# Kernel tuning notes

Measured on AMD Instinct MI355X. Metric: run time of the kernel, lower is better.

## Reference

```python
import jax, jax.numpy as jnp
import numpy as np

PATCH_WEIGHT = 0.5  # module init kwarg
B, C, H = 2, 4, 128  # vol dims (H=W=D)
N, P = 128, 32       # num patches total, patch edge (Hp=Wp=Dp)


def setup_inputs() -> dict:
    key = jax.random.key(0)
    k1, k2, k3 = jax.random.split(key, 3)
    patches = jax.random.normal(k1, (N, C, P, P, P), dtype=jnp.float32)
    vol = jax.random.normal(k2, (B, C, H, H, H), dtype=jnp.float32)
    # lower bound in [0, H-P] so the PxPxP slice stays in-bounds; center = lower + P//2
    crop_centers = jax.random.randint(k3, (N, 3), 0, H - P + 1, dtype=jnp.int32) + P // 2
    return {"patches": patches, "vol": vol, "crop_centers": crop_centers}


def reference(patches, vol, crop_centers):
    n, c_dim, p = patches.shape[0], patches.shape[1], patches.shape[2]
    b_dim = vol.shape[0]
    num_patch_per_batch = n // b_dim
    b_idx = jnp.arange(n) // num_patch_per_batch            # [N] batch index per patch
    lo = crop_centers - p // 2                              # [N,3] slice lower bounds
    offs = jnp.arange(p)
    hi = lo[:, 0, None] + offs                              # [N,P]
    wi = lo[:, 1, None] + offs                              # [N,P]
    di = lo[:, 2, None] + offs                              # [N,P]
    c_idx = jnp.arange(c_dim)
    # module: new_vol = vol*(1-pw); w_t is overwritten with ones, so add pw*patch
    new_vol = vol * (1.0 - PATCH_WEIGHT)
    new_vol = new_vol.at[
        b_idx[:, None, None, None, None],
        c_idx[None, :, None, None, None],
        hi[:, None, :, None, None],
        wi[:, None, None, :, None],
        di[:, None, None, None, :],
    ].add(patches * PATCH_WEIGHT)                           # scatter-add handles overlaps
    return new_vol
```

## Files before the change

### kernel.cpp

```cpp
#include <hip/hip_runtime.h>


#define PW 0.5f
constexpr int C = 4, H = 128, P = 32;
constexpr int NPB = 64;
constexpr int PCH = P * P * P;

__global__ __launch_bounds__(256) void patch_gather_kernel(
        const float* __restrict__ patches,
        const int*   __restrict__ centers,
        const float4* __restrict__ vol4,
        float4* __restrict__ out4) {
    __shared__ int s_list[NPB];
    __shared__ int s_n;

    int blk = blockIdx.x;
    int b   = blk >> 11;
    int blo = blk & 2047;
    int tid = threadIdx.x;

    int h  = blo >> 4;
    int w0 = (blo << 3) & 127;

    if (tid < 64) {
        int pn  = tid;
        int lo0 = centers[(b * NPB + pn) * 3 + 0] - 16;
        int lo1 = centers[(b * NPB + pn) * 3 + 1] - 16;
        int lo2 = centers[(b * NPB + pn) * 3 + 2] - 16;
        bool hit = ((unsigned)(h - lo0) < P) &&
                   ((unsigned)(w0 - lo1 + 7) < (P + 7));
        unsigned long long m = __ballot(hit);
        if (hit) {
            int pos = __popcll(m & ((1ull << tid) - 1ull));
            s_list[pos] = (pn << 21) | (lo0 << 14) | (lo1 << 7) | lo2;
        }
        if (tid == 0) s_n = __popcll(m);
    }
    __syncthreads();

    int d0 = (tid & 31) * 4;
    int w  = w0 + (tid >> 5);

    float acc[C][4] = {};
    int nh = s_n;
    const float* pbatch = patches + (size_t)b * NPB * C * PCH;

    for (int i = 0; i < nh; ++i) {
        int e   = s_list[i];
        int pn  = e >> 21;
        int lo1 = (e >> 7) & 127;
        unsigned wi = (unsigned)(w - lo1);
        if (wi < P) {
            int lo0 = (e >> 14) & 127;
            int lo2 = e & 127;
            int hi  = h - lo0;
            int k0  = d0 - lo2;
            if (k0 > -4 && k0 < P) {
                const float* pb = pbatch + (size_t)pn * C * PCH
                                + hi * (P * P) + wi * P;
                #pragma unroll
                for (int e4 = 0; e4 < 4; ++e4) {
                    int k = k0 + e4;
                    if ((unsigned)k < P) {
                        #pragma unroll
                        for (int c = 0; c < C; ++c)
                            acc[c][e4] += pb[c * PCH + k];
                    }
                }
            }
        }
    }

    #pragma unroll
    for (int c = 0; c < C; ++c) {
        int idx4 = ((((b * C + c) * H + h) * H + w) * H + d0) >> 2;
        float4 v = vol4[idx4];
        float4 o;
        o.x = v.x * (1.0f - PW) + acc[c][0] * PW;
        o.y = v.y * (1.0f - PW) + acc[c][1] * PW;
        o.z = v.z * (1.0f - PW) + acc[c][2] * PW;
        o.w = v.w * (1.0f - PW) + acc[c][3] * PW;
        out4[idx4] = o;
    }
}

extern "C" void kernel_launch(void* const* d_in, const int* in_sizes, int n_in,
                              void* d_out, int out_size, void* d_ws, size_t ws_size,
                              hipStream_t stream) {
    const float* patches = (const float*)d_in[0];
    const float* vol     = (const float*)d_in[1];
    const int*   centers = (const int*)d_in[2];
    float* out = (float*)d_out;

    patch_gather_kernel<<<4096, 256, 0, stream>>>(
        patches, centers, (const float4*)vol, (float4*)out);
}
```

Measured before the change: 53.63 us.

## Scatter patch rows into shared-memory accumulator with float4 loads and LDS atomics

Instead of each thread scanning every hit patch and doing scalar, divergent gathers, each hit patch's overlapping rows are loaded with coalesced float4 reads and scattered into a per-block shared-memory accumulator using LDS atomicAdd. The patch list entries now carry precomputed h/w offsets and width count so only overlapping rows are processed. Volume loads are issued early to overlap with the scatter phase. This adds a shared-memory zeroing pass, an extra barrier, and LDS atomic contention on unaligned d offsets.

```diff
diff --git a/kernel.cpp b/kernel.cpp
--- a/kernel.cpp
+++ b/kernel.cpp
@@ -1,16 +1,16 @@
 #include <hip/hip_runtime.h>
 
 
-#define PW 0.5f
-constexpr int C = 4, H = 128, P = 32;
 constexpr int NPB = 64;
-constexpr int PCH = P * P * P;
+constexpr int CH4 = 128 * 128 * 32;
+constexpr int PCH4 = 32 * 32 * 8;
 
 __global__ __launch_bounds__(256) void patch_gather_kernel(
-        const float* __restrict__ patches,
+        const float4* __restrict__ patches4,
         const int*   __restrict__ centers,
         const float4* __restrict__ vol4,
         float4* __restrict__ out4) {
+    __shared__ float s_acc[4 * 8 * 128];
     __shared__ int s_list[NPB];
     __shared__ int s_n;
 
@@ -22,65 +22,73 @@
     int h  = blo >> 4;
     int w0 = (blo << 3) & 127;
 
+    int base4 = (((b * 4) * 128 + h) * 128 + (w0 + (tid >> 5))) * 32 + (tid & 31);
+    float4 v0 = vol4[base4];
+    float4 v1 = vol4[base4 + CH4];
+    float4 v2 = vol4[base4 + 2 * CH4];
+    float4 v3 = vol4[base4 + 3 * CH4];
+
+    float4* sa4 = (float4*)s_acc;
+    #pragma unroll
+    for (int j = 0; j < 4; ++j)
+        sa4[tid + j * 256] = make_float4(0.f, 0.f, 0.f, 0.f);
+
     if (tid < 64) {
-        int pn  = tid;
-        int lo0 = centers[(b * NPB + pn) * 3 + 0] - 16;
-        int lo1 = centers[(b * NPB + pn) * 3 + 1] - 16;
-        int lo2 = centers[(b * NPB + pn) * 3 + 2] - 16;
-        bool hit = ((unsigned)(h - lo0) < P) &&
-                   ((unsigned)(w0 - lo1 + 7) < (P + 7));
+        int lo0 = centers[(b * NPB + tid) * 3 + 0] - 16;
+        int lo1 = centers[(b * NPB + tid) * 3 + 1] - 16;
+        int lo2 = centers[(b * NPB + tid) * 3 + 2] - 16;
+        int wlo = max(lo1, w0), whi = min(lo1 + 31, w0 + 7);
+        int nw = whi - wlo + 1;
+        bool hit = ((unsigned)(h - lo0) < 32u) && (nw > 0);
         unsigned long long m = __ballot(hit);
         if (hit) {
             int pos = __popcll(m & ((1ull << tid) - 1ull));
-            s_list[pos] = (pn << 21) | (lo0 << 14) | (lo1 << 7) | lo2;
+            int hi = h - lo0;
+            int wi0 = wlo - lo1;
+            int wOff = wlo - w0;
+            s_list[pos] = (tid << 24) | (hi << 19) | (lo2 << 12) |
+                          (wi0 << 7) | (wOff << 4) | nw;
         }
         if (tid == 0) s_n = __popcll(m);
     }
     __syncthreads();
 
-    int d0 = (tid & 31) * 4;
-    int w  = w0 + (tid >> 5);
-
-    float acc[C][4] = {};
     int nh = s_n;
-    const float* pbatch = patches + (size_t)b * NPB * C * PCH;
-
+    const float4* pbase = patches4 + (size_t)b * NPB * 4 * PCH4;
     for (int i = 0; i < nh; ++i) {
-        int e   = s_list[i];
-        int pn  = e >> 21;
-        int lo1 = (e >> 7) & 127;
-        unsigned wi = (unsigned)(w - lo1);
-        if (wi < P) {
-            int lo0 = (e >> 14) & 127;
-            int lo2 = e & 127;
-            int hi  = h - lo0;
-            int k0  = d0 - lo2;
-            if (k0 > -4 && k0 < P) {
-                const float* pb = pbatch + (size_t)pn * C * PCH
-                                + hi * (P * P) + wi * P;
-                #pragma unroll
-                for (int e4 = 0; e4 < 4; ++e4) {
-                    int k = k0 + e4;
-                    if ((unsigned)k < P) {
-                        #pragma unroll
-                        for (int c = 0; c < C; ++c)
-                            acc[c][e4] += pb[c * PCH + k];
-                    }
-                }
-            }
+        int e  = s_list[i];
+        int nw = e & 15;
+        if (tid < (nw << 5)) {
+            int k4   = tid & 7;
+            int c    = (tid >> 3) & 3;
+            int woff = tid >> 5;
+            int pn   = e >> 24;
+            int hi   = (e >> 19) & 31;
+            int lo2  = (e >> 12) & 127;
+            int wi0  = (e >> 7) & 31;
+            int wOff = (e >> 4) & 7;
+            float4 pv = pbase[(size_t)(pn * 4 + c) * PCH4 +
+                              (hi * 32 + wi0 + woff) * 8 + k4];
+            float* a = &s_acc[(c * 8 + wOff + woff) * 128 + lo2 + (k4 << 2)];
+            atomicAdd(a + 0, pv.x);
+            atomicAdd(a + 1, pv.y);
+            atomicAdd(a + 2, pv.z);
+            atomicAdd(a + 3, pv.w);
         }
     }
+    __syncthreads();
 
+    int l4 = (tid >> 5) * 32 + (tid & 31);
     #pragma unroll
-    for (int c = 0; c < C; ++c) {
-        int idx4 = ((((b * C + c) * H + h) * H + w) * H + d0) >> 2;
-        float4 v = vol4[idx4];
+    for (int c = 0; c < 4; ++c) {
+        float4 acc = sa4[c * 256 + l4];
+        float4 v = (c == 0) ? v0 : (c == 1) ? v1 : (c == 2) ? v2 : v3;
         float4 o;
-        o.x = v.x * (1.0f - PW) + acc[c][0] * PW;
-        o.y = v.y * (1.0f - PW) + acc[c][1] * PW;
-        o.z = v.z * (1.0f - PW) + acc[c][2] * PW;
-        o.w = v.w * (1.0f - PW) + acc[c][3] * PW;
-        out4[idx4] = o;
+        o.x = (v.x + acc.x) * 0.5f;
+        o.y = (v.y + acc.y) * 0.5f;
+        o.z = (v.z + acc.z) * 0.5f;
+        o.w = (v.w + acc.w) * 0.5f;
+        out4[base4 + c * CH4] = o;
     }
 }
 
@@ -93,5 +101,5 @@
     float* out = (float*)d_out;
 
     patch_gather_kernel<<<4096, 256, 0, stream>>>(
-        patches, centers, (const float4*)vol, (float4*)out);
+        (const float4*)patches, centers, (const float4*)vol, (float4*)out);
 }
```

Result: slower. 175.0 us (+226.3%).
